# Performance work log

Measured on AMD Instinct MI355X. Metric: run time of the kernel, lower is better.

## Reference

```python
import jax, jax.numpy as jnp
import numpy as np

HIDDEN = 64
N_HEADS = 4
TOP_K = 10
ALPHA = 0.3


def setup_inputs() -> dict:
    key = jax.random.key(0)
    ks = jax.random.split(key, 12)
    B, N, T, Dd, Ds, H = 4, 2048, 32, 16, 8, HIDDEN
    s = lambda i, shape, scale: (jax.random.normal(ks[i], shape, dtype=jnp.float32) * scale)
    return {
        "x_dyn": jax.random.normal(ks[0], (B, N, T, Dd), dtype=jnp.float32),
        "x_stat": jax.random.normal(ks[1], (B, N, Ds), dtype=jnp.float32),
        "A_prior": jax.random.uniform(ks[2], (B, N, N), dtype=jnp.float32),
        "W_dyn": s(3, (Dd, H), 1.0 / np.sqrt(Dd)),
        "b_dyn": jnp.zeros((H,), jnp.float32),
        "W_stat": s(4, (Ds, H), 1.0 / np.sqrt(Ds)),
        "b_stat": jnp.zeros((H,), jnp.float32),
        "W_fuse": s(5, (2 * H, H), 1.0 / np.sqrt(2 * H)),
        "b_fuse": jnp.zeros((H,), jnp.float32),
        "Wq": s(6, (H, H), 1.0 / np.sqrt(H)),
        "Wk": s(7, (H, H), 1.0 / np.sqrt(H)),
    }


def reference(x_dyn, x_stat, A_prior, W_dyn, b_dyn, W_stat, b_stat, W_fuse, b_fuse, Wq, Wk):
    B, N = x_dyn.shape[0], x_dyn.shape[1]
    H, nh = HIDDEN, N_HEADS
    dh = H // nh

    # TemporalEncoder: linear + mean over time + ReLU -> (B, N, H)
    h = jax.nn.relu(jnp.mean(x_dyn @ W_dyn + b_dyn, axis=2))
    # FeatureEncoder: linear + ReLU -> (B, N, H)
    h_s = jax.nn.relu(x_stat @ W_stat + b_stat)
    # Fusion
    h = jnp.concatenate([h, h_s], axis=-1) @ W_fuse + b_fuse

    # GraphAttention: multi-head softmax(QK^T / sqrt(dh)) averaged over heads
    q = (h @ Wq).reshape(B, N, nh, dh)
    k = (h @ Wk).reshape(B, N, nh, dh)
    scores = jnp.einsum("bnhd,bmhd->bhnm", q, k) / jnp.sqrt(jnp.float32(dh))
    A_learn = jnp.mean(jax.nn.softmax(scores, axis=-1), axis=1)  # (B, N, N)

    # Top-k mask along last dim (scatter 1s at topk indices)
    _, topk_inds = jax.lax.top_k(A_learn, TOP_K)  # (B, N, k)
    b_idx = jnp.arange(B)[:, None, None]
    n_idx = jnp.arange(N)[None, :, None]
    mask = jnp.zeros_like(A_learn).at[b_idx, n_idx, topk_inds].set(1.0)
    A_sparse = A_learn * mask
    A_learn = (A_sparse + jnp.swapaxes(A_sparse, 1, 2)) * 0.5

    # Blend with prior
    A_final = ALPHA * A_prior + (1.0 - ALPHA) * A_learn

    # Laplacian L = D - A
    degree = jnp.sum(A_final, axis=-1)  # (B, N)
    eye = jnp.eye(N, dtype=A_final.dtype)
    L = degree[..., None] * eye - A_final
    return (L, A_final)
```

## Files before the change

kernel.cpp:

```cpp
#include <hip/hip_runtime.h>

#define NBATCH 4
#define NN 2048
#define NR 8192
#define TOPK 10

typedef __attribute__((ext_vector_type(4))) float f32x4;
typedef __attribute__((ext_vector_type(8))) short bf16x8;

__device__ inline unsigned short f2bf(float x) {
    unsigned u = __float_as_uint(x);
    unsigned r = (u + 0x7FFF + ((u >> 16) & 1)) >> 16;
    return (unsigned short)r;
}

__global__ __launch_bounds__(256) void k1_encode(
    const float* __restrict__ xd, const float* __restrict__ xs,
    const float* __restrict__ Wd, const float* __restrict__ bd,
    const float* __restrict__ Ws, const float* __restrict__ bs,
    const float* __restrict__ Wf, const float* __restrict__ bf,
    const float* __restrict__ Wq, const float* __restrict__ Wk,
    unsigned short* __restrict__ qh, unsigned short* __restrict__ kh)
{
    int wave = threadIdx.x >> 6;
    int lane = threadIdx.x & 63;
    int r = blockIdx.x * 4 + wave;

    __shared__ float xm[4][16];
    __shared__ float xst[4][8];
    __shared__ float hc[4][128];
    __shared__ float hh[4][64];

    const float* xdr = xd + (size_t)r * 512;
    float acc = 0.f;
    #pragma unroll
    for (int j = 0; j < 8; ++j) acc += xdr[lane + 64*j];
    acc += __shfl_xor(acc, 16);
    acc += __shfl_xor(acc, 32);
    if (lane < 16) xm[wave][lane] = acc * (1.0f/32.0f);
    if (lane < 8)  xst[wave][lane] = xs[(size_t)r*8 + lane];
    __syncthreads();

    float a1 = bd[lane];
    #pragma unroll
    for (int d = 0; d < 16; ++d) a1 += xm[wave][d] * Wd[d*64 + lane];
    a1 = fmaxf(a1, 0.f);
    float a2 = bs[lane];
    #pragma unroll
    for (int d = 0; d < 8; ++d) a2 += xst[wave][d] * Ws[d*64 + lane];
    a2 = fmaxf(a2, 0.f);
    hc[wave][lane] = a1;
    hc[wave][64 + lane] = a2;
    __syncthreads();

    float hv0 = bf[lane], hv1 = 0.f, hv2 = 0.f, hv3 = 0.f;
    #pragma unroll
    for (int j = 0; j < 128; j += 4) {
        hv0 += hc[wave][j]   * Wf[(j)*64   + lane];
        hv1 += hc[wave][j+1] * Wf[(j+1)*64 + lane];
        hv2 += hc[wave][j+2] * Wf[(j+2)*64 + lane];
        hv3 += hc[wave][j+3] * Wf[(j+3)*64 + lane];
    }
    hh[wave][lane] = (hv0 + hv1) + (hv2 + hv3);
    __syncthreads();

    float qv0 = 0.f, qv1 = 0.f, kv0 = 0.f, kv1 = 0.f;
    #pragma unroll
    for (int j = 0; j < 64; j += 2) {
        float h0 = hh[wave][j], h1 = hh[wave][j+1];
        qv0 += h0 * Wq[(j)*64   + lane];
        qv1 += h1 * Wq[(j+1)*64 + lane];
        kv0 += h0 * Wk[(j)*64   + lane];
        kv1 += h1 * Wk[(j+1)*64 + lane];
    }
    float qv = qv0 + qv1, kv = kv0 + kv1;
    int b = r >> 11, n = r & 2047;
    int head = lane >> 4, dim = lane & 15;
    size_t base = ((size_t)(b*4 + head) * NN + n) * 32;
    qh[base + dim] = f2bf(qv);
    qh[base + 16 + dim] = 0;
    kh[base + dim] = f2bf(kv);
    kh[base + 16 + dim] = 0;
}

__global__ __launch_bounds__(256) void k2A_stats(
    const unsigned short* __restrict__ qh, const unsigned short* __restrict__ kh,
    float* __restrict__ Mf, float* __restrict__ Rf)
{
    const float C1 = 0.36067376022224085f;
    int bh = blockIdx.x >> 7;
    int rg = blockIdx.x & 127;
    int w = threadIdx.x >> 6, l = threadIdx.x & 63;
    int quad = l >> 4, lo = l & 15;

    bf16x8 afrag = *(const bf16x8*)(qh + ((size_t)bh * NN + rg*16 + lo) * 32 + quad*8);
    const unsigned short* kbase = kh + (size_t)bh * NN * 32;

    __shared__ float redA[4][16];
    __shared__ float Mrow[16];

    float Mloc[4] = {-3e38f,-3e38f,-3e38f,-3e38f};
    for (int t = 0; t < 32; ++t) {
        int m0 = w*512 + t*16;
        bf16x8 bfrag = *(const bf16x8*)(kbase + (size_t)(m0 + lo) * 32 + quad*8);
        f32x4 acc = {0.f,0.f,0.f,0.f};
        acc = __builtin_amdgcn_mfma_f32_16x16x32_bf16(afrag, bfrag, acc, 0, 0, 0);
        #pragma unroll
        for (int rr = 0; rr < 4; ++rr) Mloc[rr] = fmaxf(Mloc[rr], acc[rr]);
    }
    #pragma unroll
    for (int d = 1; d <= 8; d <<= 1) {
        #pragma unroll
        for (int rr = 0; rr < 4; ++rr) Mloc[rr] = fmaxf(Mloc[rr], __shfl_xor(Mloc[rr], d));
    }
    if (lo == 0) {
        #pragma unroll
        for (int rr = 0; rr < 4; ++rr) redA[w][quad*4 + rr] = Mloc[rr];
    }
    __syncthreads();
    if (threadIdx.x < 16)
        Mrow[threadIdx.x] = fmaxf(fmaxf(redA[0][threadIdx.x], redA[1][threadIdx.x]),
                                  fmaxf(redA[2][threadIdx.x], redA[3][threadIdx.x]));
    __syncthreads();

    float mrr[4];
    #pragma unroll
    for (int rr = 0; rr < 4; ++rr) mrr[rr] = Mrow[quad*4 + rr];

    float Sloc[4] = {0.f,0.f,0.f,0.f};
    for (int t = 0; t < 32; ++t) {
        int m0 = w*512 + t*16;
        bf16x8 bfrag = *(const bf16x8*)(kbase + (size_t)(m0 + lo) * 32 + quad*8);
        f32x4 acc = {0.f,0.f,0.f,0.f};
        acc = __builtin_amdgcn_mfma_f32_16x16x32_bf16(afrag, bfrag, acc, 0, 0, 0);
        #pragma unroll
        for (int rr = 0; rr < 4; ++rr)
            Sloc[rr] += exp2f((acc[rr] - mrr[rr]) * C1);
    }
    #pragma unroll
    for (int d = 1; d <= 8; d <<= 1) {
        #pragma unroll
        for (int rr = 0; rr < 4; ++rr) Sloc[rr] += __shfl_xor(Sloc[rr], d);
    }
    if (lo == 0) {
        #pragma unroll
        for (int rr = 0; rr < 4; ++rr) redA[w][quad*4 + rr] = Sloc[rr];
    }
    __syncthreads();
    if (threadIdx.x < 16) {
        float S = redA[0][threadIdx.x] + redA[1][threadIdx.x]
                + redA[2][threadIdx.x] + redA[3][threadIdx.x];
        int row = rg*16 + threadIdx.x;
        Mf[(size_t)bh * NN + row] = 0.25f * Mrow[threadIdx.x];
        Rf[(size_t)bh * NN + row] = 1.0f / S;
    }
}

__global__ __launch_bounds__(256) void k2C_topk(
    const unsigned short* __restrict__ qh, const unsigned short* __restrict__ kh,
    const float* __restrict__ Mf, const float* __restrict__ Rf,
    float* __restrict__ fV, int* __restrict__ fI)
{
    const float C1 = 0.36067376022224085f;
    const float L2E = 1.4426950408889634f;
    int b  = blockIdx.x >> 7;
    int rg = blockIdx.x & 127;
    int w = threadIdx.x >> 6, l = threadIdx.x & 63;
    int quad = l >> 4, lo = l & 15;

    __shared__ unsigned short vt[16][2048];

    bf16x8 afrag[4];
    float b2[4][4], r4[4][4];
    #pragma unroll
    for (int h = 0; h < 4; ++h) {
        int bh = b*4 + h;
        afrag[h] = *(const bf16x8*)(qh + ((size_t)bh * NN + rg*16 + lo) * 32 + quad*8);
        #pragma unroll
        for (int rr = 0; rr < 4; ++rr) {
            int row = rg*16 + quad*4 + rr;
            b2[h][rr] = Mf[(size_t)bh * NN + row] * L2E;
            r4[h][rr] = Rf[(size_t)bh * NN + row] * 0.25f;
        }
    }

    int swz_w = quad << 4;
    for (int t = 0; t < 32; ++t) {
        int m0 = w*512 + t*16;
        float vacc[4] = {0.f,0.f,0.f,0.f};
        #pragma unroll
        for (int h = 0; h < 4; ++h) {
            bf16x8 bfrag = *(const bf16x8*)(kh + ((size_t)(b*4+h) * NN + m0 + lo) * 32 + quad*8);
            f32x4 acc = {0.f,0.f,0.f,0.f};
            acc = __builtin_amdgcn_mfma_f32_16x16x32_bf16(afrag[h], bfrag, acc, 0, 0, 0);
            #pragma unroll
            for (int rr = 0; rr < 4; ++rr) {
                float e = exp2f(fmaf(acc[rr], C1, -b2[h][rr]));
                vacc[rr] = fmaf(e, r4[h][rr], vacc[rr]);
            }
        }
        #pragma unroll
        for (int rr = 0; rr < 4; ++rr)
            vt[quad*4 + rr][(m0 + lo) ^ swz_w] = f2bf(vacc[rr]);
    }
    __syncthreads();

    for (int rr = 0; rr < 4; ++rr) {
        int row = w*4 + rr;
        int swz = (row >> 2) << 4;
        unsigned tk[TOPK];
        #pragma unroll
        for (int s = 0; s < TOPK; ++s) tk[s] = 0u;
        for (int j = 0; j < 16; ++j) {
            int m1 = 2*l + 128*j;
            unsigned pair = *(const unsigned*)&vt[row][m1 ^ swz];
            unsigned key0 = (pair << 16)          | (unsigned)(2047 - m1);
            unsigned key1 = (pair & 0xFFFF0000u)  | (unsigned)(2046 - m1);
            if (key0 > tk[TOPK-1]) {
                unsigned ck = key0;
                #pragma unroll
                for (int s = 0; s < TOPK; ++s) {
                    bool ins = ck > tk[s];
                    unsigned o = tk[s];
                    tk[s] = ins ? ck : o;
                    ck    = ins ? o  : ck;
                }
            }
            if (key1 > tk[TOPK-1]) {
                unsigned ck = key1;
                #pragma unroll
                for (int s = 0; s < TOPK; ++s) {
                    bool ins = ck > tk[s];
                    unsigned o = tk[s];
                    tk[s] = ins ? ck : o;
                    ck    = ins ? o  : ck;
                }
            }
        }
        int rowg = b * NN + rg*16 + row;
        #pragma unroll 1
        for (int s = 0; s < TOPK; ++s) {
            unsigned kmax = tk[0];
            #pragma unroll
            for (int d = 1; d < 64; d <<= 1) {
                unsigned o = __shfl_xor(kmax, d);
                kmax = (o > kmax) ? o : kmax;
            }
            if (tk[0] == kmax) {
                #pragma unroll
                for (int q = 0; q < TOPK-1; ++q) tk[q] = tk[q+1];
                tk[TOPK-1] = 0u;
            }
            if (l == 0) {
                fV[(size_t)s * NR + rowg] = __uint_as_float(kmax & 0xFFFF0000u);
                fI[(size_t)s * NR + rowg] = 2047 - (int)(kmax & 0x7FFu);
            }
        }
    }
}

__global__ __launch_bounds__(256) void k3_base(
    const float* __restrict__ prior, float* __restrict__ Lout,
    float* __restrict__ Aout)
{
    int r = blockIdx.x;
    const float4* pr = (const float4*)(prior + (size_t)r * NN);
    float4* Ar = (float4*)(Aout + (size_t)r * NN);
    float4* Lr = (float4*)(Lout + (size_t)r * NN);
    float sum = 0.f;
    for (int i = threadIdx.x; i < NN/4; i += 256) {
        float4 p = pr[i];
        float4 a; a.x = 0.3f*p.x; a.y = 0.3f*p.y; a.z = 0.3f*p.z; a.w = 0.3f*p.w;
        Ar[i] = a;
        float4 lv; lv.x = -a.x; lv.y = -a.y; lv.z = -a.z; lv.w = -a.w;
        Lr[i] = lv;
        sum += a.x + a.y + a.z + a.w;
    }
    #pragma unroll
    for (int o = 32; o > 0; o >>= 1) sum += __shfl_down(sum, o);
    __shared__ float wsum[4];
    if ((threadIdx.x & 63) == 0) wsum[threadIdx.x >> 6] = sum;
    __syncthreads();
    if (threadIdx.x == 0) {
        float tot = wsum[0] + wsum[1] + wsum[2] + wsum[3];
        atomicAdd(&Lout[(size_t)r * NN + (r & 2047)], tot);
    }
}

__global__ __launch_bounds__(256) void k4_scatter(
    const float* __restrict__ fV, const int* __restrict__ fI,
    float* __restrict__ Lout, float* __restrict__ Aout)
{
    int wk = blockIdx.x * 256 + threadIdx.x;
    int s = wk >> 13;
    int r = wk & 8191;
    int b = r >> 11;
    int n = r & 2047;
    float wv = 0.35f * fV[(size_t)s * NR + r];
    int j = fI[(size_t)s * NR + r];
    size_t ij = (size_t)r * NN + j;
    size_t ji = ((size_t)(b * NN + j)) * NN + n;
    atomicAdd(&Aout[ij],  wv);
    atomicAdd(&Aout[ji],  wv);
    atomicAdd(&Lout[ij], -wv);
    atomicAdd(&Lout[ji], -wv);
    atomicAdd(&Lout[((size_t)(b * NN + j)) * NN + j], wv);
    atomicAdd(&Lout[(size_t)r * NN + n],              wv);
}

extern "C" void kernel_launch(void* const* d_in, const int* in_sizes, int n_in,
                              void* d_out, int out_size, void* d_ws, size_t ws_size,
                              hipStream_t stream)
{
    const float* xd    = (const float*)d_in[0];
    const float* xs    = (const float*)d_in[1];
    const float* prior = (const float*)d_in[2];
    const float* Wd    = (const float*)d_in[3];
    const float* bd    = (const float*)d_in[4];
    const float* Ws    = (const float*)d_in[5];
    const float* bs    = (const float*)d_in[6];
    const float* Wf    = (const float*)d_in[7];
    const float* bf    = (const float*)d_in[8];
    const float* Wq    = (const float*)d_in[9];
    const float* Wk    = (const float*)d_in[10];

    float* Lout = (float*)d_out;
    float* Aout = Lout + (size_t)NR * NN;

    unsigned short* qh = (unsigned short*)d_ws;
    unsigned short* kh = qh + (size_t)16 * NN * 32;
    float* Mf  = (float*)(kh + (size_t)16 * NN * 32);
    float* Rf  = Mf + (size_t)16 * NN;
    float* fV  = Rf + (size_t)16 * NN;
    int*   fI  = (int*)(fV + (size_t)TOPK * NR);

    k1_encode<<<NR/4, 256, 0, stream>>>(xd, xs, Wd, bd, Ws, bs, Wf, bf, Wq, Wk, qh, kh);
    k2A_stats<<<16*128, 256, 0, stream>>>(qh, kh, Mf, Rf);
    k2C_topk<<<4*128, 256, 0, stream>>>(qh, kh, Mf, Rf, fV, fI);
    k3_base<<<NR, 256, 0, stream>>>(prior, Lout, Aout);
    k4_scatter<<<TOPK*NR/256, 256, 0, stream>>>(fV, fI, Lout, Aout);
}
```

Baseline: 369.7 us.

## Fuse softmax stats, top-k and scatter into one kernel without max pass

```diff
diff --git a/kernel.cpp b/kernel.cpp
--- a/kernel.cpp
+++ b/kernel.cpp
@@ -83,119 +83,116 @@
     kh[base + 16 + dim] = 0;
 }
 
-__global__ __launch_bounds__(256) void k2A_stats(
+__global__ __launch_bounds__(256) void k3_base(
+    const float* __restrict__ prior, float* __restrict__ Lout,
+    float* __restrict__ Aout)
+{
+    int r = blockIdx.x;
+    const float4* pr = (const float4*)(prior + (size_t)r * NN);
+    float4* Ar = (float4*)(Aout + (size_t)r * NN);
+    float4* Lr = (float4*)(Lout + (size_t)r * NN);
+    float sum = 0.f;
+    for (int i = threadIdx.x; i < NN/4; i += 256) {
+        float4 p = pr[i];
+        float4 a; a.x = 0.3f*p.x; a.y = 0.3f*p.y; a.z = 0.3f*p.z; a.w = 0.3f*p.w;
+        Ar[i] = a;
+        float4 lv; lv.x = -a.x; lv.y = -a.y; lv.z = -a.z; lv.w = -a.w;
+        Lr[i] = lv;
+        sum += a.x + a.y + a.z + a.w;
+    }
+    #pragma unroll
+    for (int o = 32; o > 0; o >>= 1) sum += __shfl_down(sum, o);
+    __shared__ float wsum[4];
+    if ((threadIdx.x & 63) == 0) wsum[threadIdx.x >> 6] = sum;
+    __syncthreads();
+    if (threadIdx.x == 0) {
+        float tot = wsum[0] + wsum[1] + wsum[2] + wsum[3];
+        atomicAdd(&Lout[(size_t)r * NN + (r & 2047)], tot);
+    }
+}
+
+__global__ __launch_bounds__(512) void k2_fused(
     const unsigned short* __restrict__ qh, const unsigned short* __restrict__ kh,
-    float* __restrict__ Mf, float* __restrict__ Rf)
+    float* __restrict__ Lout, float* __restrict__ Aout)
 {
     const float C1 = 0.36067376022224085f;
-    int bh = blockIdx.x >> 7;
-    int rg = blockIdx.x & 127;
-    int w = threadIdx.x >> 6, l = threadIdx.x & 63;
-    int quad = l >> 4, lo = l & 15;
-
-    bf16x8 afrag = *(const bf16x8*)(qh + ((size_t)bh * NN + rg*16 + lo) * 32 + quad*8);
-    const unsigned short* kbase = kh + (size_t)bh * NN * 32;
-
-    __shared__ float redA[4][16];
-    __shared__ float Mrow[16];
-
-    float Mloc[4] = {-3e38f,-3e38f,-3e38f,-3e38f};
-    for (int t = 0; t < 32; ++t) {
-        int m0 = w*512 + t*16;
-        bf16x8 bfrag = *(const bf16x8*)(kbase + (size_t)(m0 + lo) * 32 + quad*8);
-        f32x4 acc = {0.f,0.f,0.f,0.f};
-        acc = __builtin_amdgcn_mfma_f32_16x16x32_bf16(afrag, bfrag, acc, 0, 0, 0);
-        #pragma unroll
-        for (int rr = 0; rr < 4; ++rr) Mloc[rr] = fmaxf(Mloc[rr], acc[rr]);
-    }
-    #pragma unroll
-    for (int d = 1; d <= 8; d <<= 1) {
-        #pragma unroll
-        for (int rr = 0; rr < 4; ++rr) Mloc[rr] = fmaxf(Mloc[rr], __shfl_xor(Mloc[rr], d));
-    }
-    if (lo == 0) {
-        #pragma unroll
-        for (int rr = 0; rr < 4; ++rr) redA[w][quad*4 + rr] = Mloc[rr];
-    }
-    __syncthreads();
-    if (threadIdx.x < 16)
-        Mrow[threadIdx.x] = fmaxf(fmaxf(redA[0][threadIdx.x], redA[1][threadIdx.x]),
-                                  fmaxf(redA[2][threadIdx.x], redA[3][threadIdx.x]));
-    __syncthreads();
-
-    float mrr[4];
-    #pragma unroll
-    for (int rr = 0; rr < 4; ++rr) mrr[rr] = Mrow[quad*4 + rr];
-
-    float Sloc[4] = {0.f,0.f,0.f,0.f};
-    for (int t = 0; t < 32; ++t) {
-        int m0 = w*512 + t*16;
-        bf16x8 bfrag = *(const bf16x8*)(kbase + (size_t)(m0 + lo) * 32 + quad*8);
-        f32x4 acc = {0.f,0.f,0.f,0.f};
-        acc = __builtin_amdgcn_mfma_f32_16x16x32_bf16(afrag, bfrag, acc, 0, 0, 0);
-        #pragma unroll
-        for (int rr = 0; rr < 4; ++rr)
-            Sloc[rr] += exp2f((acc[rr] - mrr[rr]) * C1);
-    }
-    #pragma unroll
-    for (int d = 1; d <= 8; d <<= 1) {
-        #pragma unroll
-        for (int rr = 0; rr < 4; ++rr) Sloc[rr] += __shfl_xor(Sloc[rr], d);
-    }
-    if (lo == 0) {
-        #pragma unroll
-        for (int rr = 0; rr < 4; ++rr) redA[w][quad*4 + rr] = Sloc[rr];
-    }
-    __syncthreads();
-    if (threadIdx.x < 16) {
-        float S = redA[0][threadIdx.x] + redA[1][threadIdx.x]
-                + redA[2][threadIdx.x] + redA[3][threadIdx.x];
-        int row = rg*16 + threadIdx.x;
-        Mf[(size_t)bh * NN + row] = 0.25f * Mrow[threadIdx.x];
-        Rf[(size_t)bh * NN + row] = 1.0f / S;
-    }
-}
-
-__global__ __launch_bounds__(256) void k2C_topk(
-    const unsigned short* __restrict__ qh, const unsigned short* __restrict__ kh,
-    const float* __restrict__ Mf, const float* __restrict__ Rf,
-    float* __restrict__ fV, int* __restrict__ fI)
-{
-    const float C1 = 0.36067376022224085f;
-    const float L2E = 1.4426950408889634f;
     int b  = blockIdx.x >> 7;
     int rg = blockIdx.x & 127;
-    int w = threadIdx.x >> 6, l = threadIdx.x & 63;
+    int tid = threadIdx.x;
+    int w = tid >> 6, l = tid & 63;
     int quad = l >> 4, lo = l & 15;
 
     __shared__ unsigned short vt[16][2048];
+    __shared__ float redS[8][4][16];
+    __shared__ float r4s[4][16];
+    __shared__ unsigned win[16][TOPK];
 
     bf16x8 afrag[4];
-    float b2[4][4], r4[4][4];
-    #pragma unroll
-    for (int h = 0; h < 4; ++h) {
-        int bh = b*4 + h;
-        afrag[h] = *(const bf16x8*)(qh + ((size_t)bh * NN + rg*16 + lo) * 32 + quad*8);
-        #pragma unroll
-        for (int rr = 0; rr < 4; ++rr) {
-            int row = rg*16 + quad*4 + rr;
-            b2[h][rr] = Mf[(size_t)bh * NN + row] * L2E;
-            r4[h][rr] = Rf[(size_t)bh * NN + row] * 0.25f;
-        }
-    }
-
-    int swz_w = quad << 4;
-    for (int t = 0; t < 32; ++t) {
-        int m0 = w*512 + t*16;
-        float vacc[4] = {0.f,0.f,0.f,0.f};
+    #pragma unroll
+    for (int h = 0; h < 4; ++h)
+        afrag[h] = *(const bf16x8*)(qh + ((size_t)(b*4+h) * NN + rg*16 + lo) * 32 + quad*8);
+
+    float S[4][4];
+    #pragma unroll
+    for (int h = 0; h < 4; ++h)
+        #pragma unroll
+        for (int rr = 0; rr < 4; ++rr) S[h][rr] = 0.f;
+
+    for (int t = 0; t < 16; ++t) {
+        int m0 = w*256 + t*16;
         #pragma unroll
         for (int h = 0; h < 4; ++h) {
             bf16x8 bfrag = *(const bf16x8*)(kh + ((size_t)(b*4+h) * NN + m0 + lo) * 32 + quad*8);
             f32x4 acc = {0.f,0.f,0.f,0.f};
             acc = __builtin_amdgcn_mfma_f32_16x16x32_bf16(afrag[h], bfrag, acc, 0, 0, 0);
             #pragma unroll
+            for (int rr = 0; rr < 4; ++rr)
+                S[h][rr] += exp2f(acc[rr] * C1);
+        }
+    }
+    #pragma unroll
+    for (int d = 1; d <= 8; d <<= 1)
+        #pragma unroll
+        for (int h = 0; h < 4; ++h)
+            #pragma unroll
+            for (int rr = 0; rr < 4; ++rr)
+                S[h][rr] += __shfl_xor(S[h][rr], d);
+    if (lo == 0) {
+        #pragma unroll
+        for (int h = 0; h < 4; ++h)
+            #pragma unroll
+            for (int rr = 0; rr < 4; ++rr)
+                redS[w][h][quad*4 + rr] = S[h][rr];
+    }
+    __syncthreads();
+    if (tid < 64) {
+        int hh = tid >> 4, row = tid & 15;
+        float s = 0.f;
+        #pragma unroll
+        for (int ww = 0; ww < 8; ++ww) s += redS[ww][hh][row];
+        r4s[hh][row] = 0.25f / s;
+    }
+    __syncthreads();
+
+    float r4[4][4];
+    #pragma unroll
+    for (int h = 0; h < 4; ++h)
+        #pragma unroll
+        for (int rr = 0; rr < 4; ++rr)
+            r4[h][rr] = r4s[h][quad*4 + rr];
+
+    int swz_w = quad << 4;
+    for (int t = 0; t < 16; ++t) {
+        int m0 = w*256 + t*16;
+        float vacc[4] = {0.f,0.f,0.f,0.f};
+        #pragma unroll
+        for (int h = 0; h < 4; ++h) {
+            bf16x8 bfrag = *(const bf16x8*)(kh + ((size_t)(b*4+h) * NN + m0 + lo) * 32 + quad*8);
+            f32x4 acc = {0.f,0.f,0.f,0.f};
+            acc = __builtin_amdgcn_mfma_f32_16x16x32_bf16(afrag[h], bfrag, acc, 0, 0, 0);
+            #pragma unroll
             for (int rr = 0; rr < 4; ++rr) {
-                float e = exp2f(fmaf(acc[rr], C1, -b2[h][rr]));
+                float e = exp2f(acc[rr] * C1);
                 vacc[rr] = fmaf(e, r4[h][rr], vacc[rr]);
             }
         }
@@ -205,8 +202,8 @@
     }
     __syncthreads();
 
-    for (int rr = 0; rr < 4; ++rr) {
-        int row = w*4 + rr;
+    for (int rr = 0; rr < 2; ++rr) {
+        int row = w*2 + rr;
         int swz = (row >> 2) << 4;
         unsigned tk[TOPK];
         #pragma unroll
@@ -237,7 +234,6 @@
                 }
             }
         }
-        int rowg = b * NN + rg*16 + row;
         #pragma unroll 1
         for (int s = 0; s < TOPK; ++s) {
             unsigned kmax = tk[0];
@@ -251,61 +247,26 @@
                 for (int q = 0; q < TOPK-1; ++q) tk[q] = tk[q+1];
                 tk[TOPK-1] = 0u;
             }
-            if (l == 0) {
-                fV[(size_t)s * NR + rowg] = __uint_as_float(kmax & 0xFFFF0000u);
-                fI[(size_t)s * NR + rowg] = 2047 - (int)(kmax & 0x7FFu);
-            }
-        }
-    }
-}
-
-__global__ __launch_bounds__(256) void k3_base(
-    const float* __restrict__ prior, float* __restrict__ Lout,
-    float* __restrict__ Aout)
-{
-    int r = blockIdx.x;
-    const float4* pr = (const float4*)(prior + (size_t)r * NN);
-    float4* Ar = (float4*)(Aout + (size_t)r * NN);
-    float4* Lr = (float4*)(Lout + (size_t)r * NN);
-    float sum = 0.f;
-    for (int i = threadIdx.x; i < NN/4; i += 256) {
-        float4 p = pr[i];
-        float4 a; a.x = 0.3f*p.x; a.y = 0.3f*p.y; a.z = 0.3f*p.z; a.w = 0.3f*p.w;
-        Ar[i] = a;
-        float4 lv; lv.x = -a.x; lv.y = -a.y; lv.z = -a.z; lv.w = -a.w;
-        Lr[i] = lv;
-        sum += a.x + a.y + a.z + a.w;
-    }
-    #pragma unroll
-    for (int o = 32; o > 0; o >>= 1) sum += __shfl_down(sum, o);
-    __shared__ float wsum[4];
-    if ((threadIdx.x & 63) == 0) wsum[threadIdx.x >> 6] = sum;
-    __syncthreads();
-    if (threadIdx.x == 0) {
-        float tot = wsum[0] + wsum[1] + wsum[2] + wsum[3];
-        atomicAdd(&Lout[(size_t)r * NN + (r & 2047)], tot);
-    }
-}
-
-__global__ __launch_bounds__(256) void k4_scatter(
-    const float* __restrict__ fV, const int* __restrict__ fI,
-    float* __restrict__ Lout, float* __restrict__ Aout)
-{
-    int wk = blockIdx.x * 256 + threadIdx.x;
-    int s = wk >> 13;
-    int r = wk & 8191;
-    int b = r >> 11;
-    int n = r & 2047;
-    float wv = 0.35f * fV[(size_t)s * NR + r];
-    int j = fI[(size_t)s * NR + r];
-    size_t ij = (size_t)r * NN + j;
-    size_t ji = ((size_t)(b * NN + j)) * NN + n;
-    atomicAdd(&Aout[ij],  wv);
-    atomicAdd(&Aout[ji],  wv);
-    atomicAdd(&Lout[ij], -wv);
-    atomicAdd(&Lout[ji], -wv);
-    atomicAdd(&Lout[((size_t)(b * NN + j)) * NN + j], wv);
-    atomicAdd(&Lout[(size_t)r * NN + n],              wv);
+            if (l == 0) win[row][s] = kmax;
+        }
+    }
+    __syncthreads();
+
+    if (tid < 16*TOPK) {
+        int row = tid / TOPK, s = tid % TOPK;
+        unsigned key = win[row][s];
+        float wv = 0.35f * __uint_as_float(key & 0xFFFF0000u);
+        int j = 2047 - (int)(key & 0x7FFu);
+        int n = rg*16 + row;
+        size_t rbase = (size_t)(b*NN + n) * NN;
+        size_t jbase = (size_t)(b*NN + j) * NN;
+        atomicAdd(&Aout[rbase + j],  wv);
+        atomicAdd(&Aout[jbase + n],  wv);
+        atomicAdd(&Lout[rbase + j], -wv);
+        atomicAdd(&Lout[jbase + n], -wv);
+        atomicAdd(&Lout[jbase + j],  wv);
+        atomicAdd(&Lout[rbase + n],  wv);
+    }
 }
 
 extern "C" void kernel_launch(void* const* d_in, const int* in_sizes, int n_in,
@@ -329,14 +290,8 @@
 
     unsigned short* qh = (unsigned short*)d_ws;
     unsigned short* kh = qh + (size_t)16 * NN * 32;
-    float* Mf  = (float*)(kh + (size_t)16 * NN * 32);
-    float* Rf  = Mf + (size_t)16 * NN;
-    float* fV  = Rf + (size_t)16 * NN;
-    int*   fI  = (int*)(fV + (size_t)TOPK * NR);
 
     k1_encode<<<NR/4, 256, 0, stream>>>(xd, xs, Wd, bd, Ws, bs, Wf, bf, Wq, Wk, qh, kh);
-    k2A_stats<<<16*128, 256, 0, stream>>>(qh, kh, Mf, Rf);
-    k2C_topk<<<4*128, 256, 0, stream>>>(qh, kh, Mf, Rf, fV, fI);
     k3_base<<<NR, 256, 0, stream>>>(prior, Lout, Aout);
-    k4_scatter<<<TOPK*NR/256, 256, 0, stream>>>(fV, fI, Lout, Aout);
-}
+    k2_fused<<<NBATCH*128, 512, 0, stream>>>(qh, kh, Lout, Aout);
+}
```

After: 385.0 us. 4.1% more time.
